# Kernel optimization log

Hardware: AMD Instinct MI355X
Metric: run time of the kernel (lower is better)

## Reference

```python
import jax, jax.numpy as jnp
import numpy as np

B, D_MODEL, N, H = 4, 256, 2048, 4
DIM = D_MODEL // H  # 64


def setup_inputs() -> dict:
    k = jax.random.key(0)
    ks = jax.random.split(k, 11)
    mk = lambda kk, shape, s=1.0: jax.random.normal(kk, shape, dtype=jnp.float32) * s
    return {
        'query': mk(ks[0], (B, D_MODEL, N)),
        'key': mk(ks[1], (B, D_MODEL, N)),
        'value': mk(ks[2], (B, D_MODEL, N)),
        # 1x1 Conv1d == per-position linear: weight [out, in], bias [out]
        'wq': mk(ks[3], (D_MODEL, D_MODEL), 0.05), 'bq': mk(ks[4], (D_MODEL,), 0.05),
        'wk': mk(ks[5], (D_MODEL, D_MODEL), 0.05), 'bk': mk(ks[6], (D_MODEL,), 0.05),
        'wv': mk(ks[7], (D_MODEL, D_MODEL), 0.05), 'bv': mk(ks[8], (D_MODEL,), 0.05),
        'wm': mk(ks[9], (D_MODEL, D_MODEL), 0.05), 'bm': mk(ks[10], (D_MODEL,), 0.05),
    }


def _proj(x, w, b):
    # Conv1d(kernel_size=1): [b, c_in, n] -> [b, c_out, n]
    return jnp.einsum('oc,bcn->bon', w, x) + b[None, :, None]


def reference(query, key, value, wq, bq, wk, bk, wv, bv, wm, bm):
    b = query.shape[0]
    # project and split channels d_model -> (dim, h); matches torch .view(b, dim, h, -1)
    q = _proj(query, wq, bq).reshape(b, DIM, H, -1)
    kk = _proj(key, wk, bk).reshape(b, DIM, H, -1)
    v = _proj(value, wv, bv).reshape(b, DIM, H, -1)
    scores = jnp.einsum('bdhn,bdhm->bhnm', q, kk) / jnp.sqrt(jnp.float32(DIM))
    prob = jax.nn.softmax(scores, axis=-1)  # [b, h, n, m]
    x = jnp.einsum('bhnm,bdhm->bdhn', prob, v)
    return _proj(x.reshape(b, DIM * H, -1), wm, bm)
```

## Files before the change

### kernel.cpp

```cpp
#include <hip/hip_runtime.h>
#include <hip/hip_bf16.h>

#define DMODEL 256
#define NSEQ   2048
#define NB     4
#define NH     4
#define DHEAD  64

typedef __attribute__((ext_vector_type(8))) short short8;
typedef __attribute__((ext_vector_type(4))) float float4v;
typedef __attribute__((ext_vector_type(2))) unsigned int uint2v;
typedef unsigned short u16;

#define AS1 __attribute__((address_space(1)))
#define AS3 __attribute__((address_space(3)))

static __device__ inline u16 f2bf(float f) {
    unsigned u = __builtin_bit_cast(unsigned, f);
    u += 0x7fffu + ((u >> 16) & 1u);
    return (u16)(u >> 16);
}
static __device__ inline unsigned pack2bf(float a, float b) {
    return (unsigned)f2bf(a) | ((unsigned)f2bf(b) << 16);
}
static __device__ inline float max3f(float a, float b, float c) {
    return fmaxf(fmaxf(a, b), c);
}
static __device__ inline float tmax16(const float4v* s) {
    float a = max3f(s[0][0], s[0][1], s[0][2]);
    float b = max3f(s[0][3], s[1][0], s[1][1]);
    float c = max3f(s[1][2], s[1][3], s[2][0]);
    float d = max3f(s[2][1], s[2][2], s[2][3]);
    float e = max3f(s[3][0], s[3][1], s[3][2]);
    float f = max3f(a, b, c);
    float g = max3f(d, e, s[3][3]);
    return fmaxf(f, g);
}

__global__ __launch_bounds__(256) void prep_kernel(
    const float* __restrict__ xq, const float* __restrict__ xk,
    const float* __restrict__ xv,
    const float* __restrict__ wq, const float* __restrict__ wk,
    const float* __restrict__ wv, const float* __restrict__ wm,
    u16* __restrict__ xt_ws, u16* __restrict__ wbf)
{
    const int bid = blockIdx.x;
    const int tid = threadIdx.x;

    if (bid >= 1536) {
        const int id = bid - 1536;
        const int sr = id & 255, m = id >> 8;
        const float* W = (m == 0) ? wq : (m == 1) ? wk : (m == 2) ? wv : wm;
        float v;
        if (m < 3) {
            int og = (sr & ~15) | ((sr & 3) << 2) | ((sr >> 2) & 3);
            v = W[(size_t)og * DMODEL + tid];
        } else {
            int c = ((tid & 63) << 2) | (tid >> 6);
            v = W[(size_t)sr * DMODEL + c];
        }
        wbf[(size_t)m * 65536 + (size_t)sr * DMODEL + tid] = f2bf(v);
        return;
    }

    const int nt = bid & 31;
    const int ct = (bid >> 5) & 3;
    const int z  = bid >> 7;
    const int b = z / 3, mode = z % 3;
    const float* X = ((mode == 0) ? xq : (mode == 1) ? xk : xv) + (size_t)b * DMODEL * NSEQ;
    u16* dst = xt_ws + (size_t)z * NSEQ * DMODEL;

    __shared__ u16 t[64][72];

    #pragma unroll
    for (int i = 0; i < 4; i++) {
        int e = tid + i * 256;
        int c = e >> 4;
        int n4 = (e & 15) * 4;
        float4v v = *(const float4v*)&X[(size_t)(ct * 64 + c) * NSEQ + nt * 64 + n4];
        #pragma unroll
        for (int j = 0; j < 4; j++) {
            int row = n4 + j;
            int fr = (row & 7) ^ ((row >> 3) & 7);
            t[row][(((c >> 3) ^ fr) << 3) + (c & 7)] = f2bf(v[j]);
        }
    }
    __syncthreads();
    #pragma unroll
    for (int i = 0; i < 4; i++) {
        int e = tid + i * 256;
        int n = e >> 4;
        int cb = (e & 15) * 4;
        int fr = (n & 7) ^ ((n >> 3) & 7);
        uint2v val = *(const uint2v*)&t[n][(((cb >> 3) ^ fr) << 3) + (cb & 7)];
        *(uint2v*)&dst[(size_t)(nt * 64 + n) * DMODEL + ct * 64 + cb] = val;
    }
}

__global__ __launch_bounds__(256) void proj_qkv_kernel(
    const u16* __restrict__ xt_ws, const u16* __restrict__ wbf,
    const float* __restrict__ bqp, const float* __restrict__ bkp, const float* __restrict__ bvp,
    u16* __restrict__ q_ws, u16* __restrict__ k_ws, u16* __restrict__ vt_ws)
{
    const int nt0 = blockIdx.x, ot = blockIdx.y, bz = blockIdx.z;
    const int b = bz / 3, mode = bz % 3;
    const float* BI = (mode == 0) ? bqp : (mode == 1) ? bkp : bvp;

    const int tid = threadIdx.x;
    const int wave = tid >> 6, lane = tid & 63;
    const int g = lane >> 4, ql = lane & 15;
    const int srow8 = lane >> 3, su = lane & 7;
    const int u_l = su ^ srow8;
    const int obase = ot * 64, nbase = nt0 * 64;

    const u16* Asrc = wbf + (size_t)mode * 65536;
    const u16* Bsrc = xt_ws + (size_t)bz * (NSEQ * DMODEL);

    __shared__ u16 at[2][64][64];
    __shared__ u16 bt[2][64][64];

    float4v acc[4];
    #pragma unroll
    for (int i = 0; i < 4; i++) acc[i] = (float4v){0.f, 0.f, 0.f, 0.f};

    #define PSTAGE(bufi_, c0_)                                                         \
        { _Pragma("unroll")                                                            \
          for (int p_ = 0; p_ < 2; p_++) {                                             \
            int rb_ = wave * 8 + p_ * 32;                                              \
            int row_ = rb_ + srow8;                                                    \
            __builtin_amdgcn_global_load_lds(                                          \
                (const AS1 unsigned int*)(Asrc + (size_t)(obase + row_) * DMODEL + (c0_) + u_l * 8), \
                (AS3 unsigned int*)&at[bufi_][rb_][0], 16, 0, 0);                      \
            __builtin_amdgcn_global_load_lds(                                          \
                (const AS1 unsigned int*)(Bsrc + (size_t)(nbase + row_) * DMODEL + (c0_) + u_l * 8), \
                (AS3 unsigned int*)&bt[bufi_][rb_][0], 16, 0, 0);                      \
          } }

    PSTAGE(0, 0)
    __syncthreads();
    int buf = 0;
    const int sw = ql & 7;
    #pragma unroll
    for (int t = 0; t < 4; t++) {
        if (t < 3) PSTAGE(buf ^ 1, (t + 1) * 64)
        #pragma unroll
        for (int kc = 0; kc < 2; kc++) {
            short8 afrag = *(const short8*)&at[buf][wave * 16 + ql][(((kc * 4 + g) ^ sw)) * 8];
            #pragma unroll
            for (int nt = 0; nt < 4; nt++) {
                short8 bfrag = *(const short8*)&bt[buf][nt * 16 + ql][(((kc * 4 + g) ^ sw)) * 8];
                acc[nt] = __builtin_amdgcn_mfma_f32_16x16x32_bf16(afrag, bfrag, acc[nt], 0, 0, 0);
            }
        }
        __syncthreads();
        buf ^= 1;
    }
    #undef PSTAGE

    const int h = g;
    const int d0 = (obase + wave * 16) >> 2;
    float bias[4];
    #pragma unroll
    for (int r = 0; r < 4; r++) bias[r] = BI[obase + wave * 16 + 4 * r + g];

    #pragma unroll
    for (int nt = 0; nt < 4; nt++) {
        int n = nbase + nt * 16 + ql;
        float v[4];
        #pragma unroll
        for (int r = 0; r < 4; r++) v[r] = acc[nt][r] + bias[r];
        if (mode == 0) {
            #pragma unroll
            for (int r = 0; r < 4; r++) v[r] *= 0.18033688011112042f;
            uint2v pk = {pack2bf(v[0], v[1]), pack2bf(v[2], v[3])};
            *(uint2v*)&q_ws[((size_t)(b * NH + h) * NSEQ + n) * DHEAD + d0] = pk;
        } else if (mode == 1) {
            uint2v pk = {pack2bf(v[0], v[1]), pack2bf(v[2], v[3])};
            *(uint2v*)&k_ws[((size_t)(b * NH + h) * NSEQ + n) * DHEAD + d0] = pk;
        } else {
            #pragma unroll
            for (int r = 0; r < 4; r++)
                vt_ws[((size_t)(b * NH + h) * DHEAD + d0 + r) * NSEQ + n] = f2bf(v[r]);
        }
    }
}

__global__ __launch_bounds__(512) void attn_kernel(
    const u16* __restrict__ q_ws, const u16* __restrict__ k_ws,
    const u16* __restrict__ vt_ws, u16* __restrict__ x_hs)
{
    const int bid = blockIdx.x;
    const int orig = (bid & 7) * 32 + (bid >> 3);
    const int bh = orig >> 4;
    const int qt128 = orig & 15;
    const int tid = threadIdx.x;
    const int wave = tid >> 6, lane = tid & 63;
    const int g = lane >> 4, ql = lane & 15;
    const int qbase = qt128 * 128 + wave * 16;

    const u16* qp = q_ws + ((size_t)bh * NSEQ + qbase) * DHEAD;
    const u16* kp = k_ws + (size_t)bh * NSEQ * DHEAD;
    const u16* vp = vt_ws + (size_t)bh * DHEAD * NSEQ;

    __shared__ u16 kt[2][64][64];
    __shared__ u16 vt[2][64][64];
    __shared__ u16 p_lds[8][16][72];

    const int srow = lane >> 3;
    const int su_l = lane & 7;
    const int u_l  = su_l ^ srow;
    const int swz  = ql & 7;

    short8 qf[2];
    #pragma unroll
    for (int kc = 0; kc < 2; kc++)
        qf[kc] = *(const short8*)(qp + (size_t)ql * DHEAD + kc * 32 + g * 8);

    float4v acc[4];
    #pragma unroll
    for (int t = 0; t < 4; t++) acc[t] = (float4v){0.f, 0.f, 0.f, 0.f};
    float mrun = -INFINITY, lrun = 0.f;

    #define STAGE(mb_, bufi_)                                                          \
        {                                                                              \
            int row_ = wave * 8 + srow;                                                \
            __builtin_amdgcn_global_load_lds(                                          \
                (const AS1 unsigned int*)(kp + (size_t)((mb_) + row_) * DHEAD + u_l * 8), \
                (AS3 unsigned int*)&kt[bufi_][wave * 8][0], 16, 0, 0);                 \
            __builtin_amdgcn_global_load_lds(                                          \
                (const AS1 unsigned int*)(vp + (size_t)row_ * NSEQ + (mb_) + u_l * 8), \
                (AS3 unsigned int*)&vt[bufi_][wave * 8][0], 16, 0, 0);                 \
        }

    STAGE(0, 0);
    __syncthreads();

    int buf = 0;
    for (int t = 0; t < NSEQ / 64; t++) {
        const int mb = t * 64;
        if (t < NSEQ / 64 - 1) STAGE(mb + 64, buf ^ 1);

        float4v st[4];
        #pragma unroll
        for (int mt = 0; mt < 4; mt++) st[mt] = (float4v){0.f, 0.f, 0.f, 0.f};
        #pragma unroll
        for (int mt = 0; mt < 4; mt++) {
            #pragma unroll
            for (int kc = 0; kc < 2; kc++) {
                short8 kf = *(const short8*)&kt[buf][mt * 16 + ql][((kc * 4 + g) ^ swz) * 8];
                st[mt] = __builtin_amdgcn_mfma_f32_16x16x32_bf16(kf, qf[kc], st[mt], 0, 0, 0);
            }
        }

        float tmax = tmax16(&st[0]);
        tmax = fmaxf(tmax, __shfl_xor(tmax, 16, 64));
        tmax = fmaxf(tmax, __shfl_xor(tmax, 32, 64));

        if (__any(tmax > mrun + 8.f)) {
            float mnew = fmaxf(mrun, tmax);
            float a = __builtin_amdgcn_exp2f(mrun - mnew);
            #pragma unroll
            for (int tt = 0; tt < 4; tt++)
                #pragma unroll
                for (int r = 0; r < 4; r++) acc[tt][r] *= a;
            lrun *= a;
            mrun = mnew;
        }

        float psum = 0.f;
        #pragma unroll
        for (int mt = 0; mt < 4; mt++) {
            float p0 = __builtin_amdgcn_exp2f(st[mt][0] - mrun);
            float p1 = __builtin_amdgcn_exp2f(st[mt][1] - mrun);
            float p2 = __builtin_amdgcn_exp2f(st[mt][2] - mrun);
            float p3 = __builtin_amdgcn_exp2f(st[mt][3] - mrun);
            psum += (p0 + p1) + (p2 + p3);
            *(uint2v*)&p_lds[wave][ql][mt * 16 + g * 4] = (uint2v){pack2bf(p0, p1), pack2bf(p2, p3)};
        }
        psum += __shfl_xor(psum, 16, 64);
        psum += __shfl_xor(psum, 32, 64);
        lrun += psum;

        #pragma unroll
        for (int kc = 0; kc < 2; kc++) {
            short8 pf = *(const short8*)&p_lds[wave][ql][kc * 32 + g * 8];
            #pragma unroll
            for (int tt = 0; tt < 4; tt++) {
                short8 vf = *(const short8*)&vt[buf][tt * 16 + ql][((kc * 4 + g) ^ swz) * 8];
                acc[tt] = __builtin_amdgcn_mfma_f32_16x16x32_bf16(vf, pf, acc[tt], 0, 0, 0);
            }
        }
        __syncthreads();
        buf ^= 1;
    }
    #undef STAGE

    float inv = 1.f / lrun;
    u16* xrow = x_hs + ((size_t)bh * NSEQ + qbase + ql) * DHEAD;
    #pragma unroll
    for (int t = 0; t < 4; t++) {
        uint2v pk = {pack2bf(acc[t][0] * inv, acc[t][1] * inv),
                     pack2bf(acc[t][2] * inv, acc[t][3] * inv)};
        *(uint2v*)&xrow[t * 16 + g * 4] = pk;
    }
}

__global__ __launch_bounds__(256) void proj_out_kernel(
    const u16* __restrict__ x_hs, const u16* __restrict__ wbf,
    const float* __restrict__ bm, float* __restrict__ out)
{
    const int nt0 = blockIdx.x, ot = blockIdx.y, b = blockIdx.z;

    const int tid = threadIdx.x;
    const int wave = tid >> 6, lane = tid & 63;
    const int g = lane >> 4, ql = lane & 15;
    const int srow8 = lane >> 3, su = lane & 7;
    const int u_l = su ^ srow8;
    const int obase = ot * 64, nbase = nt0 * 64;

    const u16* Asrc = wbf + (size_t)3 * 65536;

    __shared__ u16 at[2][64][64];
    __shared__ u16 bt[2][64][64];

    float4v acc[4];
    #pragma unroll
    for (int i = 0; i < 4; i++) acc[i] = (float4v){0.f, 0.f, 0.f, 0.f};

    #define OSTAGE(bufi_, c0_)                                                         \
        { _Pragma("unroll")                                                            \
          for (int p_ = 0; p_ < 2; p_++) {                                             \
            int rb_ = wave * 8 + p_ * 32;                                              \
            int row_ = rb_ + srow8;                                                    \
            __builtin_amdgcn_global_load_lds(                                          \
                (const AS1 unsigned int*)(Asrc + (size_t)(obase + row_) * DMODEL + (c0_) + u_l * 8), \
                (AS3 unsigned int*)&at[bufi_][rb_][0], 16, 0, 0);                      \
            __builtin_amdgcn_global_load_lds(                                          \
                (const AS1 unsigned int*)(x_hs + ((size_t)(b * NH + ((c0_) >> 6)) * NSEQ + nbase + row_) * DHEAD + u_l * 8), \
                (AS3 unsigned int*)&bt[bufi_][rb_][0], 16, 0, 0);                      \
          } }

    OSTAGE(0, 0)
    __syncthreads();
    int buf = 0;
    const int sw = ql & 7;
    #pragma unroll
    for (int t = 0; t < 4; t++) {
        if (t < 3) OSTAGE(buf ^ 1, (t + 1) * 64)
        #pragma unroll
        for (int kc = 0; kc < 2; kc++) {
            short8 afrag = *(const short8*)&at[buf][wave * 16 + ql][(((kc * 4 + g) ^ sw)) * 8];
            #pragma unroll
            for (int nt = 0; nt < 4; nt++) {
                short8 bfrag = *(const short8*)&bt[buf][nt * 16 + ql][(((kc * 4 + g) ^ sw)) * 8];
                acc[nt] = __builtin_amdgcn_mfma_f32_16x16x32_bf16(afrag, bfrag, acc[nt], 0, 0, 0);
            }
        }
        __syncthreads();
        buf ^= 1;
    }
    #undef OSTAGE

    const int o0 = obase + wave * 16 + g * 4;
    #pragma unroll
    for (int nt = 0; nt < 4; nt++) {
        int n = nbase + nt * 16 + ql;
        #pragma unroll
        for (int r = 0; r < 4; r++) {
            int o = o0 + r;
            out[((size_t)b * DMODEL + o) * NSEQ + n] = acc[nt][r] + bm[o];
        }
    }
}

extern "C" void kernel_launch(void* const* d_in, const int* in_sizes, int n_in,
                              void* d_out, int out_size, void* d_ws, size_t ws_size,
                              hipStream_t stream)
{
    const float* query = (const float*)d_in[0];
    const float* key   = (const float*)d_in[1];
    const float* value = (const float*)d_in[2];
    const float* wq = (const float*)d_in[3];
    const float* bq = (const float*)d_in[4];
    const float* wk = (const float*)d_in[5];
    const float* bk = (const float*)d_in[6];
    const float* wv = (const float*)d_in[7];
    const float* bv = (const float*)d_in[8];
    const float* wm = (const float*)d_in[9];
    const float* bm = (const float*)d_in[10];
    float* out = (float*)d_out;

    char* ws = (char*)d_ws;
    const size_t SEG = (size_t)NB * NH * NSEQ * DHEAD * sizeof(u16);
    u16* q_ws  = (u16*)(ws);
    u16* k_ws  = (u16*)(ws + SEG);
    u16* vt_ws = (u16*)(ws + 2 * SEG);
    u16* x_hs  = (u16*)(ws + 3 * SEG);
    u16* xt_ws = (u16*)(ws + 4 * SEG);
    u16* wbf   = (u16*)(ws + 4 * SEG + (size_t)12 * NSEQ * DMODEL * sizeof(u16));

    prep_kernel<<<dim3(2560), 256, 0, stream>>>(
        query, key, value, wq, wk, wv, wm, xt_ws, wbf);
    proj_qkv_kernel<<<dim3(32, 4, 12), 256, 0, stream>>>(
        xt_ws, wbf, bq, bk, bv, q_ws, k_ws, vt_ws);
    attn_kernel<<<dim3(256), 512, 0, stream>>>(q_ws, k_ws, vt_ws, x_hs);
    proj_out_kernel<<<dim3(32, 4, NB), 256, 0, stream>>>(x_hs, wbf, bm, out);
}
```

Baseline: 155.3 us.

## Split attention over key halves and merge partials in output projection

Each query tile's key range is split into two halves, doubling the attention grid to 512 blocks so more CUs are occupied. Each half writes unnormalized fp32 accumulators plus running max and sum, and the output projection kernel merges the two halves (flash-decoding style rescale) while staging its B operand into LDS. This trades higher partial-result traffic, more workspace and a loss of double buffering in proj_out for better parallelism in the attention kernel.

```diff
diff --git a/kernel.cpp b/kernel.cpp
--- a/kernel.cpp
+++ b/kernel.cpp
@@ -9,6 +9,7 @@
 
 typedef __attribute__((ext_vector_type(8))) short short8;
 typedef __attribute__((ext_vector_type(4))) float float4v;
+typedef __attribute__((ext_vector_type(2))) float float2v;
 typedef __attribute__((ext_vector_type(2))) unsigned int uint2v;
 typedef unsigned short u16;
 
@@ -187,20 +188,23 @@
 
 __global__ __launch_bounds__(512) void attn_kernel(
     const u16* __restrict__ q_ws, const u16* __restrict__ k_ws,
-    const u16* __restrict__ vt_ws, u16* __restrict__ x_hs)
+    const u16* __restrict__ vt_ws, float* __restrict__ part_ws,
+    float* __restrict__ ml_ws)
 {
     const int bid = blockIdx.x;
-    const int orig = (bid & 7) * 32 + (bid >> 3);
-    const int bh = orig >> 4;
-    const int qt128 = orig & 15;
+    const int orig = (bid & 7) * 64 + (bid >> 3);
+    const int bh = orig >> 5;
+    const int qt128 = (orig >> 1) & 15;
+    const int half = orig & 1;
     const int tid = threadIdx.x;
     const int wave = tid >> 6, lane = tid & 63;
     const int g = lane >> 4, ql = lane & 15;
     const int qbase = qt128 * 128 + wave * 16;
 
     const u16* qp = q_ws + ((size_t)bh * NSEQ + qbase) * DHEAD;
-    const u16* kp = k_ws + (size_t)bh * NSEQ * DHEAD;
+    const u16* kp = k_ws + (size_t)bh * NSEQ * DHEAD + (size_t)half * 1024 * DHEAD;
     const u16* vp = vt_ws + (size_t)bh * DHEAD * NSEQ;
+    const int voff = half * 1024;
 
     __shared__ u16 kt[2][64][64];
     __shared__ u16 vt[2][64][64];
@@ -228,7 +232,7 @@
                 (const AS1 unsigned int*)(kp + (size_t)((mb_) + row_) * DHEAD + u_l * 8), \
                 (AS3 unsigned int*)&kt[bufi_][wave * 8][0], 16, 0, 0);                 \
             __builtin_amdgcn_global_load_lds(                                          \
-                (const AS1 unsigned int*)(vp + (size_t)row_ * NSEQ + (mb_) + u_l * 8), \
+                (const AS1 unsigned int*)(vp + (size_t)row_ * NSEQ + voff + (mb_) + u_l * 8), \
                 (AS3 unsigned int*)&vt[bufi_][wave * 8][0], 16, 0, 0);                 \
         }
 
@@ -236,9 +240,9 @@
     __syncthreads();
 
     int buf = 0;
-    for (int t = 0; t < NSEQ / 64; t++) {
+    for (int t = 0; t < 16; t++) {
         const int mb = t * 64;
-        if (t < NSEQ / 64 - 1) STAGE(mb + 64, buf ^ 1);
+        if (t < 15) STAGE(mb + 64, buf ^ 1);
 
         float4v st[4];
         #pragma unroll
@@ -295,19 +299,20 @@
     }
     #undef STAGE
 
-    float inv = 1.f / lrun;
-    u16* xrow = x_hs + ((size_t)bh * NSEQ + qbase + ql) * DHEAD;
-    #pragma unroll
-    for (int t = 0; t < 4; t++) {
-        uint2v pk = {pack2bf(acc[t][0] * inv, acc[t][1] * inv),
-                     pack2bf(acc[t][2] * inv, acc[t][3] * inv)};
-        *(uint2v*)&xrow[t * 16 + g * 4] = pk;
+    float* prow = part_ws + ((size_t)(half * 16 + bh) * NSEQ + qbase + ql) * 64;
+    #pragma unroll
+    for (int t = 0; t < 4; t++)
+        *(float4v*)&prow[t * 16 + g * 4] = acc[t];
+    if (g == 0) {
+        *(float2v*)&ml_ws[((size_t)(half * 16 + bh) * NSEQ + qbase + ql) * 2] =
+            (float2v){mrun, lrun};
     }
 }
 
 __global__ __launch_bounds__(256) void proj_out_kernel(
-    const u16* __restrict__ x_hs, const u16* __restrict__ wbf,
-    const float* __restrict__ bm, float* __restrict__ out)
+    const float* __restrict__ part_ws, const float* __restrict__ ml_ws,
+    const u16* __restrict__ wbf, const float* __restrict__ bm,
+    float* __restrict__ out)
 {
     const int nt0 = blockIdx.x, ot = blockIdx.y, b = blockIdx.z;
 
@@ -320,46 +325,65 @@
 
     const u16* Asrc = wbf + (size_t)3 * 65536;
 
-    __shared__ u16 at[2][64][64];
-    __shared__ u16 bt[2][64][64];
+    __shared__ u16 at[64][64];
+    __shared__ u16 bt[64][64];
 
     float4v acc[4];
     #pragma unroll
     for (int i = 0; i < 4; i++) acc[i] = (float4v){0.f, 0.f, 0.f, 0.f};
 
-    #define OSTAGE(bufi_, c0_)                                                         \
-        { _Pragma("unroll")                                                            \
-          for (int p_ = 0; p_ < 2; p_++) {                                             \
-            int rb_ = wave * 8 + p_ * 32;                                              \
-            int row_ = rb_ + srow8;                                                    \
-            __builtin_amdgcn_global_load_lds(                                          \
-                (const AS1 unsigned int*)(Asrc + (size_t)(obase + row_) * DMODEL + (c0_) + u_l * 8), \
-                (AS3 unsigned int*)&at[bufi_][rb_][0], 16, 0, 0);                      \
-            __builtin_amdgcn_global_load_lds(                                          \
-                (const AS1 unsigned int*)(x_hs + ((size_t)(b * NH + ((c0_) >> 6)) * NSEQ + nbase + row_) * DHEAD + u_l * 8), \
-                (AS3 unsigned int*)&bt[bufi_][rb_][0], 16, 0, 0);                      \
-          } }
-
-    OSTAGE(0, 0)
-    __syncthreads();
-    int buf = 0;
+    const int rrow = tid >> 2;
+    const int qcol = tid & 3;
     const int sw = ql & 7;
+
     #pragma unroll
     for (int t = 0; t < 4; t++) {
-        if (t < 3) OSTAGE(buf ^ 1, (t + 1) * 64)
+        const int c0 = t * 64;
+        __syncthreads();
+        #pragma unroll
+        for (int p_ = 0; p_ < 2; p_++) {
+            int rb_ = wave * 8 + p_ * 32;
+            int row_ = rb_ + srow8;
+            __builtin_amdgcn_global_load_lds(
+                (const AS1 unsigned int*)(Asrc + (size_t)(obase + row_) * DMODEL + c0 + u_l * 8),
+                (AS3 unsigned int*)&at[rb_][0], 16, 0, 0);
+        }
+        {
+            const int bh = b * NH + t;
+            const int n = nbase + rrow;
+            const float* p0 = part_ws + ((size_t)bh * NSEQ + n) * 64;
+            const float* p1 = part_ws + ((size_t)(16 + bh) * NSEQ + n) * 64;
+            float2v ml0 = *(const float2v*)&ml_ws[((size_t)bh * NSEQ + n) * 2];
+            float2v ml1 = *(const float2v*)&ml_ws[((size_t)(16 + bh) * NSEQ + n) * 2];
+            float mM = fmaxf(ml0[0], ml1[0]);
+            float e0 = __builtin_amdgcn_exp2f(ml0[0] - mM);
+            float e1 = __builtin_amdgcn_exp2f(ml1[0] - mM);
+            float inv = 1.f / (ml0[1] * e0 + ml1[1] * e1);
+            float s0 = e0 * inv, s1 = e1 * inv;
+            #pragma unroll
+            for (int j = 0; j < 4; j++) {
+                int cb = qcol * 16 + j * 4;
+                float4v f0 = *(const float4v*)&p0[cb];
+                float4v f1 = *(const float4v*)&p1[cb];
+                float x0 = f0[0] * s0 + f1[0] * s1;
+                float x1 = f0[1] * s0 + f1[1] * s1;
+                float x2 = f0[2] * s0 + f1[2] * s1;
+                float x3 = f0[3] * s0 + f1[3] * s1;
+                *(uint2v*)&bt[rrow][(((cb >> 3) ^ (rrow & 7)) << 3) + (cb & 7)] =
+                    (uint2v){pack2bf(x0, x1), pack2bf(x2, x3)};
+            }
+        }
+        __syncthreads();
         #pragma unroll
         for (int kc = 0; kc < 2; kc++) {
-            short8 afrag = *(const short8*)&at[buf][wave * 16 + ql][(((kc * 4 + g) ^ sw)) * 8];
+            short8 afrag = *(const short8*)&at[wave * 16 + ql][(((kc * 4 + g) ^ sw)) * 8];
             #pragma unroll
             for (int nt = 0; nt < 4; nt++) {
-                short8 bfrag = *(const short8*)&bt[buf][nt * 16 + ql][(((kc * 4 + g) ^ sw)) * 8];
+                short8 bfrag = *(const short8*)&bt[nt * 16 + ql][(((kc * 4 + g) ^ sw)) * 8];
                 acc[nt] = __builtin_amdgcn_mfma_f32_16x16x32_bf16(afrag, bfrag, acc[nt], 0, 0, 0);
             }
         }
-        __syncthreads();
-        buf ^= 1;
-    }
-    #undef OSTAGE
+    }
 
     const int o0 = obase + wave * 16 + g * 4;
     #pragma unroll
@@ -392,17 +416,20 @@
 
     char* ws = (char*)d_ws;
     const size_t SEG = (size_t)NB * NH * NSEQ * DHEAD * sizeof(u16);
-    u16* q_ws  = (u16*)(ws);
-    u16* k_ws  = (u16*)(ws + SEG);
-    u16* vt_ws = (u16*)(ws + 2 * SEG);
-    u16* x_hs  = (u16*)(ws + 3 * SEG);
-    u16* xt_ws = (u16*)(ws + 4 * SEG);
-    u16* wbf   = (u16*)(ws + 4 * SEG + (size_t)12 * NSEQ * DMODEL * sizeof(u16));
+    u16*   q_ws    = (u16*)(ws);
+    u16*   k_ws    = (u16*)(ws + SEG);
+    u16*   vt_ws   = (u16*)(ws + 2 * SEG);
+    float* part_ws = (float*)(ws + 3 * SEG);
+    float* ml_ws   = (float*)(ws + 3 * SEG + (size_t)2 * 16 * NSEQ * 64 * sizeof(float));
+    char*  after_ml = ws + 3 * SEG + (size_t)2 * 16 * NSEQ * 64 * sizeof(float)
+                         + (size_t)2 * 16 * NSEQ * 2 * sizeof(float);
+    u16*   xt_ws   = (u16*)(after_ml);
+    u16*   wbf     = (u16*)(after_ml + (size_t)12 * NSEQ * DMODEL * sizeof(u16));
 
     prep_kernel<<<dim3(2560), 256, 0, stream>>>(
         query, key, value, wq, wk, wv, wm, xt_ws, wbf);
     proj_qkv_kernel<<<dim3(32, 4, 12), 256, 0, stream>>>(
         xt_ws, wbf, bq, bk, bv, q_ws, k_ws, vt_ws);
-    attn_kernel<<<dim3(256), 512, 0, stream>>>(q_ws, k_ws, vt_ws, x_hs);
-    proj_out_kernel<<<dim3(32, 4, NB), 256, 0, stream>>>(x_hs, wbf, bm, out);
-}
+    attn_kernel<<<dim3(512), 512, 0, stream>>>(q_ws, k_ws, vt_ws, part_ws, ml_ws);
+    proj_out_kernel<<<dim3(32, 4, NB), 256, 0, stream>>>(part_ws, ml_ws, wbf, bm, out);
+}
```

Measured after the change: 146.4 us. 1.06x faster.
